# Kernel tuning notes

Hardware: AMD Instinct MI355X
Metric: run time of the kernel (lower is better)

## Reference

```python
import jax, jax.numpy as jnp
import numpy as np

BN_EPS = 1e-5


def conv1d(x, w, pad):
    # x: [N, Cin, L], w: [Cout, Cin, K] -> [N, Cout, L]
    return jax.lax.conv_general_dilated(
        x, w, window_strides=(1,), padding=[(pad, pad)],
        dimension_numbers=("NCH", "OIH", "NCH"))


def setup_inputs() -> dict:
    key = jax.random.key(0)
    k1, k2, k3, k4 = jax.random.split(key, 4)
    b, c, h, w = 32, 512, 64, 64
    x = jax.random.normal(k1, (b, c, h, w), jnp.float32)
    # ECA-style channel conv: kernel_size=5 for channel=512
    w1 = jax.random.normal(k2, (1, 1, 5), jnp.float32) * 0.3
    # Spatial convs created in forward: Conv1d(h,h,3) and Conv1d(w,w,3)
    wh = jax.random.normal(k3, (h, h, 3), jnp.float32) * (1.0 / np.sqrt(3.0 * h))
    ww = jax.random.normal(k4, (w, w, 3), jnp.float32) * (1.0 / np.sqrt(3.0 * w))
    gamma = jnp.ones((1,), jnp.float32)
    beta = jnp.zeros((1,), jnp.float32)
    return {"x": x, "w1": w1, "wh": wh, "ww": ww, "gamma": gamma, "beta": beta}


def reference(x, w1, wh, ww, gamma, beta):
    b, c, h, w = x.shape
    # Channel attention: global avg pool -> conv1d over channel axis -> sigmoid
    f1 = jnp.mean(x, axis=(2, 3)).reshape(b, 1, c)          # [b,1,c]
    f1 = conv1d(f1, w1, pad=2).reshape(b, c, 1, 1)
    f1 = jax.nn.sigmoid(f1)
    F = x * f1
    # Spatial attention: channel-mean -> conv1d along w (channels=h) + conv1d along h (channels=w)
    f2 = jnp.mean(x, axis=1)                                 # [b,h,w]
    f2_h = conv1d(f2, wh, pad=1).reshape(b, 1, h, w)
    f2_w = conv1d(jnp.transpose(f2, (0, 2, 1)), ww, pad=1)   # [b,w,h]
    f2_w = jnp.transpose(f2_w, (0, 2, 1)).reshape(b, 1, h, w)
    f2 = f2_h + f2_w
    # BatchNorm2d(1), training-mode batch statistics over (b, h, w)
    mu = jnp.mean(f2)
    var = jnp.mean(jnp.square(f2 - mu))
    f2 = gamma[0] * (f2 - mu) * jax.lax.rsqrt(var + BN_EPS) + beta[0]
    return F * jax.nn.sigmoid(f2)
```

## Files before the change

kernel.cpp:

```cpp
#include <hip/hip_runtime.h>

#define NB 32
#define NC 512
#define NH 64
#define NW 64
#define NHW 4096
#define NTOT ((size_t)NB * NC * NHW)

typedef float f32x4 __attribute__((ext_vector_type(4)));

#define OFF_S1PART 0
#define OFF_F2PART 262144
#define OFF_F1SIG  1310720
#define OFF_F2RAW  1327104
#define OFF_BNPART 1458176

__global__ __launch_bounds__(256) void k_reduce(const float* __restrict__ x,
                                                float* __restrict__ s1part,
                                                float* __restrict__ f2part) {
  __shared__ f32x4 comb[4][64];
  const int bid = blockIdx.x;
  const int jc = bid & 15;
  const int cg = (bid >> 4) & 7;
  const int b = bid >> 7;
  const int tid = threadIdx.x;
  const int lane = tid & 63;
  const int wv = tid >> 6;

  const size_t base =
      ((size_t)(b * NC + cg * 64 + wv * 16)) * NHW + jc * 256 + lane * 4;
  f32x4 p = {0.f, 0.f, 0.f, 0.f};
  float myS = 0.f;
#pragma unroll
  for (int k = 0; k < 16; ++k) {
    const f32x4 v = *reinterpret_cast<const f32x4*>(x + base + (size_t)k * NHW);
    p += v;
    float s = (v.x + v.y) + (v.z + v.w);
#pragma unroll
    for (int m = 32; m > 0; m >>= 1) s += __shfl_xor(s, m);
    myS = (lane == k) ? s : myS;
  }
  if (lane < 16)
    s1part[(size_t)(b * NC + cg * 64 + wv * 16 + lane) * 16 + jc] = myS;

  comb[wv][lane] = p;
  __syncthreads();
  if (tid < 64) {
    const f32x4 r =
        (comb[0][tid] + comb[1][tid]) + (comb[2][tid] + comb[3][tid]);
    reinterpret_cast<f32x4*>(f2part)[((size_t)cg * NB + b) * 1024 + jc * 64 +
                                     tid] = r;
  }
}

__global__ __launch_bounds__(256) void k_f2(const float* __restrict__ f2part,
                                            const float* __restrict__ s1part,
                                            const float* __restrict__ w1,
                                            const float* __restrict__ wh,
                                            const float* __restrict__ ww,
                                            float* __restrict__ f2raw,
                                            float* __restrict__ bnpart,
                                            float* __restrict__ f1sig) {
  __shared__ float mp[66][66];
  __shared__ float wwL[64][193];
  __shared__ float red[8];
  const int b = blockIdx.x >> 4;
  const int rg = blockIdx.x & 15;
  const int tid = threadIdx.x;

  if (tid < 66) {
    mp[0][tid] = 0.f;
    mp[65][tid] = 0.f;
    mp[tid][0] = 0.f;
    mp[tid][65] = 0.f;
  }
  for (int t = tid; t < 64 * 192; t += 256) wwL[t / 192][t % 192] = ww[t];
#pragma unroll
  for (int t4 = tid; t4 < 1024; t4 += 256) {
    f32x4 s = {0.f, 0.f, 0.f, 0.f};
#pragma unroll
    for (int cg = 0; cg < 8; ++cg)
      s += reinterpret_cast<const f32x4*>(f2part +
                                          ((size_t)(cg * NB + b)) * NHW)[t4];
    s *= (1.0f / (float)NC);
    const int r = t4 >> 4;
    const int c = (t4 & 15) * 4;
    mp[1 + r][1 + c + 0] = s.x;
    mp[1 + r][1 + c + 1] = s.y;
    mp[1 + r][1 + c + 2] = s.z;
    mp[1 + r][1 + c + 3] = s.w;
  }
  __syncthreads();

  const int i = rg * 4 + (tid >> 6);
  const int j = tid & 63;
  const float* whp = wh + 192 * __builtin_amdgcn_readfirstlane(i);
  const float* wwp = &wwL[j][0];
  float acc = 0.f;
#pragma unroll 16
  for (int ic = 0; ic < 64; ++ic) {
    acc += whp[ic * 3 + 0] * mp[ic + 1][j] +
           whp[ic * 3 + 1] * mp[ic + 1][j + 1] +
           whp[ic * 3 + 2] * mp[ic + 1][j + 2];
    acc += wwp[ic * 3 + 0] * mp[i][ic + 1] +
           wwp[ic * 3 + 1] * mp[i + 1][ic + 1] +
           wwp[ic * 3 + 2] * mp[i + 2][ic + 1];
  }
  f2raw[(size_t)b * NHW + (i << 6) + j] = acc;

  float lsum = acc, lsq = acc * acc;
#pragma unroll
  for (int off = 32; off > 0; off >>= 1) {
    lsum += __shfl_down(lsum, off);
    lsq += __shfl_down(lsq, off);
  }
  if ((tid & 63) == 0) {
    red[(tid >> 6) * 2 + 0] = lsum;
    red[(tid >> 6) * 2 + 1] = lsq;
  }
  __syncthreads();
  if (tid == 0) {
    bnpart[blockIdx.x * 2 + 0] = red[0] + red[2] + red[4] + red[6];
    bnpart[blockIdx.x * 2 + 1] = red[1] + red[3] + red[5] + red[7];
  }

  if (rg == 0) {
#pragma unroll
    for (int c0 = 0; c0 < 512; c0 += 256) {
      const int c = c0 + tid;
      float acc5 = 0.f;
#pragma unroll
      for (int k = 0; k < 5; ++k) {
        const int cc = c + k - 2;
        if (cc >= 0 && cc < NC) {
          const f32x4* sp =
              reinterpret_cast<const f32x4*>(s1part + (size_t)(b * NC + cc) * 16);
          const f32x4 a = (sp[0] + sp[1]) + (sp[2] + sp[3]);
          acc5 += w1[k] * ((a.x + a.y) + (a.z + a.w));
        }
      }
      acc5 *= (1.0f / (float)NHW);
      f1sig[b * NC + c] = 1.0f / (1.0f + __expf(-acc5));
    }
  }
}

__global__ __launch_bounds__(256) void k_out(const float* __restrict__ x,
                                             const float* __restrict__ f1sig,
                                             const float* __restrict__ f2raw,
                                             const float* __restrict__ bnpart,
                                             const float* __restrict__ gamma,
                                             const float* __restrict__ beta,
                                             float* __restrict__ out) {
  __shared__ float bnv[2];
  const int tid = threadIdx.x;
  if (tid < 64) {
    float s = 0.f, q = 0.f;
#pragma unroll
    for (int r = 0; r < 8; ++r) {
      s += bnpart[2 * (tid + 64 * r) + 0];
      q += bnpart[2 * (tid + 64 * r) + 1];
    }
#pragma unroll
    for (int off = 32; off > 0; off >>= 1) {
      s += __shfl_down(s, off);
      q += __shfl_down(q, off);
    }
    if (tid == 0) {
      const float N = (float)(NB * NHW);
      const float mu = s / N;
      const float var = q / N - mu * mu;
      bnv[0] = mu;
      bnv[1] = gamma[0] * rsqrtf(var + 1e-5f);
    }
  }
  __syncthreads();
  const float mu = bnv[0];
  const float g = bnv[1];
  const float bt = beta[0];

  const int grp = blockIdx.x >> 3;
  const int bid = (511 - grp) * 8 + (blockIdx.x & 7);
  const int jc = bid & 15;
  const int cg = (bid >> 4) & 7;
  const int b = bid >> 7;
  const int lane = tid & 63;
  const int wv = tid >> 6;

  const int px = jc * 256 + lane * 4;
  const f32x4 fv = *reinterpret_cast<const f32x4*>(f2raw + b * NHW + px);
  f32x4 s2;
  s2.x = 1.0f / (1.0f + __expf(-(g * (fv.x - mu) + bt)));
  s2.y = 1.0f / (1.0f + __expf(-(g * (fv.y - mu) + bt)));
  s2.z = 1.0f / (1.0f + __expf(-(g * (fv.z - mu) + bt)));
  s2.w = 1.0f / (1.0f + __expf(-(g * (fv.w - mu) + bt)));

  const int cbase = __builtin_amdgcn_readfirstlane(b * NC + cg * 64 + wv * 16);
  float f1v[16];
#pragma unroll
  for (int k = 0; k < 16; ++k) f1v[k] = f1sig[cbase + k];

  const size_t base = (size_t)cbase * NHW + px;
#pragma unroll
  for (int k = 0; k < 16; ++k) {
    const f32x4 xv = *reinterpret_cast<const f32x4*>(x + base + (size_t)k * NHW);
    const f32x4 ov = xv * (s2 * f1v[k]);
    __builtin_nontemporal_store(
        ov, reinterpret_cast<f32x4*>(out + base + (size_t)k * NHW));
  }
}

extern "C" void kernel_launch(void* const* d_in, const int* in_sizes, int n_in,
                              void* d_out, int out_size, void* d_ws,
                              size_t ws_size, hipStream_t stream) {
  const float* x = (const float*)d_in[0];
  const float* w1 = (const float*)d_in[1];
  const float* wh = (const float*)d_in[2];
  const float* ww = (const float*)d_in[3];
  const float* gamma = (const float*)d_in[4];
  const float* beta = (const float*)d_in[5];
  float* out = (float*)d_out;
  float* ws = (float*)d_ws;

  float* s1part = ws + OFF_S1PART;
  float* f2part = ws + OFF_F2PART;
  float* f1sig = ws + OFF_F1SIG;
  float* f2raw = ws + OFF_F2RAW;
  float* bnpart = ws + OFF_BNPART;

  k_reduce<<<NB * 8 * 16, 256, 0, stream>>>(x, s1part, f2part);
  k_f2<<<NB * 16, 256, 0, stream>>>(f2part, s1part, w1, wh, ww, f2raw, bnpart,
                                    f1sig);
  k_out<<<NB * 8 * 16, 256, 0, stream>>>(x, f1sig, f2raw, bnpart, gamma, beta,
                                         out);
}
```

Baseline: 146.8 us.

## Replace per-channel shuffle reductions with LDS transpose; compute two rows per thread in spatial conv

In the reduce kernel, the per-channel spatial sums no longer use a 6-step butterfly shuffle for each of 16 channels. Each lane's partial sums are staged in padded shared memory and then reduced cooperatively, 4 lanes per channel. The spatial conv kernel now computes two output rows per thread and reuses the loaded map and weight values across both rows, which halves the grid to 256 blocks and shrinks the BN partial count to match. Costs are extra LDS traffic and footprint in the reduce kernel, and fewer blocks for the small conv kernel.

```diff
diff --git a/kernel.cpp b/kernel.cpp
--- a/kernel.cpp
+++ b/kernel.cpp
@@ -18,6 +18,7 @@
 __global__ __launch_bounds__(256) void k_reduce(const float* __restrict__ x,
                                                 float* __restrict__ s1part,
                                                 float* __restrict__ f2part) {
+  __shared__ float sbuf[4][16][65];
   __shared__ f32x4 comb[4][64];
   const int bid = blockIdx.x;
   const int jc = bid & 15;
@@ -30,21 +31,27 @@
   const size_t base =
       ((size_t)(b * NC + cg * 64 + wv * 16)) * NHW + jc * 256 + lane * 4;
   f32x4 p = {0.f, 0.f, 0.f, 0.f};
-  float myS = 0.f;
 #pragma unroll
   for (int k = 0; k < 16; ++k) {
     const f32x4 v = *reinterpret_cast<const f32x4*>(x + base + (size_t)k * NHW);
     p += v;
-    float s = (v.x + v.y) + (v.z + v.w);
-#pragma unroll
-    for (int m = 32; m > 0; m >>= 1) s += __shfl_xor(s, m);
-    myS = (lane == k) ? s : myS;
-  }
-  if (lane < 16)
-    s1part[(size_t)(b * NC + cg * 64 + wv * 16 + lane) * 16 + jc] = myS;
-
+    sbuf[wv][k][lane] = (v.x + v.y) + (v.z + v.w);
+  }
   comb[wv][lane] = p;
   __syncthreads();
+
+  {
+    const int c = lane >> 2;
+    const int seg = (lane & 3) * 16;
+    float t = 0.f;
+#pragma unroll
+    for (int m = 0; m < 16; ++m) t += sbuf[wv][c][seg + m];
+    t += __shfl_xor(t, 1);
+    t += __shfl_xor(t, 2);
+    if ((lane & 3) == 0)
+      s1part[(size_t)(b * NC + cg * 64 + wv * 16 + c) * 16 + jc] = t;
+  }
+
   if (tid < 64) {
     const f32x4 r =
         (comb[0][tid] + comb[1][tid]) + (comb[2][tid] + comb[3][tid]);
@@ -64,8 +71,8 @@
   __shared__ float mp[66][66];
   __shared__ float wwL[64][193];
   __shared__ float red[8];
-  const int b = blockIdx.x >> 4;
-  const int rg = blockIdx.x & 15;
+  const int b = blockIdx.x >> 3;
+  const int rg = blockIdx.x & 7;
   const int tid = threadIdx.x;
 
   if (tid < 66) {
@@ -92,23 +99,35 @@
   }
   __syncthreads();
 
-  const int i = rg * 4 + (tid >> 6);
   const int j = tid & 63;
-  const float* whp = wh + 192 * __builtin_amdgcn_readfirstlane(i);
+  const int iA = rg * 8 + (tid >> 6) * 2;
+  const int iB = iA + 1;
+  const float* whA = wh + 192 * __builtin_amdgcn_readfirstlane(iA);
+  const float* whB = whA + 192;
   const float* wwp = &wwL[j][0];
-  float acc = 0.f;
-#pragma unroll 16
+  float accA = 0.f, accB = 0.f;
+#pragma unroll 8
   for (int ic = 0; ic < 64; ++ic) {
-    acc += whp[ic * 3 + 0] * mp[ic + 1][j] +
-           whp[ic * 3 + 1] * mp[ic + 1][j + 1] +
-           whp[ic * 3 + 2] * mp[ic + 1][j + 2];
-    acc += wwp[ic * 3 + 0] * mp[i][ic + 1] +
-           wwp[ic * 3 + 1] * mp[i + 1][ic + 1] +
-           wwp[ic * 3 + 2] * mp[i + 2][ic + 1];
-  }
-  f2raw[(size_t)b * NHW + (i << 6) + j] = acc;
-
-  float lsum = acc, lsq = acc * acc;
+    const float m0 = mp[ic + 1][j];
+    const float m1 = mp[ic + 1][j + 1];
+    const float m2 = mp[ic + 1][j + 2];
+    accA += whA[ic * 3 + 0] * m0 + whA[ic * 3 + 1] * m1 + whA[ic * 3 + 2] * m2;
+    accB += whB[ic * 3 + 0] * m0 + whB[ic * 3 + 1] * m1 + whB[ic * 3 + 2] * m2;
+    const float w0 = wwp[ic * 3 + 0];
+    const float w1v = wwp[ic * 3 + 1];
+    const float w2 = wwp[ic * 3 + 2];
+    const float r0 = mp[iA][ic + 1];
+    const float r1 = mp[iA + 1][ic + 1];
+    const float r2 = mp[iA + 2][ic + 1];
+    const float r3 = mp[iA + 3][ic + 1];
+    accA += w0 * r0 + w1v * r1 + w2 * r2;
+    accB += w0 * r1 + w1v * r2 + w2 * r3;
+  }
+  f2raw[(size_t)b * NHW + (iA << 6) + j] = accA;
+  f2raw[(size_t)b * NHW + (iB << 6) + j] = accB;
+
+  float lsum = accA + accB;
+  float lsq = accA * accA + accB * accB;
 #pragma unroll
   for (int off = 32; off > 0; off >>= 1) {
     lsum += __shfl_down(lsum, off);
@@ -133,8 +152,8 @@
       for (int k = 0; k < 5; ++k) {
         const int cc = c + k - 2;
         if (cc >= 0 && cc < NC) {
-          const f32x4* sp =
-              reinterpret_cast<const f32x4*>(s1part + (size_t)(b * NC + cc) * 16);
+          const f32x4* sp = reinterpret_cast<const f32x4*>(
+              s1part + (size_t)(b * NC + cc) * 16);
           const f32x4 a = (sp[0] + sp[1]) + (sp[2] + sp[3]);
           acc5 += w1[k] * ((a.x + a.y) + (a.z + a.w));
         }
@@ -157,7 +176,7 @@
   if (tid < 64) {
     float s = 0.f, q = 0.f;
 #pragma unroll
-    for (int r = 0; r < 8; ++r) {
+    for (int r = 0; r < 4; ++r) {
       s += bnpart[2 * (tid + 64 * r) + 0];
       q += bnpart[2 * (tid + 64 * r) + 1];
     }
@@ -229,8 +248,8 @@
   float* bnpart = ws + OFF_BNPART;
 
   k_reduce<<<NB * 8 * 16, 256, 0, stream>>>(x, s1part, f2part);
-  k_f2<<<NB * 16, 256, 0, stream>>>(f2part, s1part, w1, wh, ww, f2raw, bnpart,
-                                    f1sig);
+  k_f2<<<NB * 8, 256, 0, stream>>>(f2part, s1part, w1, wh, ww, f2raw, bnpart,
+                                   f1sig);
   k_out<<<NB * 8 * 16, 256, 0, stream>>>(x, f1sig, f2raw, bnpart, gamma, beta,
                                          out);
 }
```

Result: no change. 145.4 us (-0.9%).
